# Kernel optimization log

Measured on AMD Instinct MI355X. Metric: run time of the kernel, lower is better.

## Reference

```python
import jax, jax.numpy as jnp
import numpy as np

HEAD_DIM = 256
L2_EPS = 1e-12  # tf.math.l2_normalize default epsilon


def setup_inputs() -> dict:
    key = jax.random.key(0)
    ks = jax.random.split(key, 6)
    B, U = 64, 2048
    D_dec, D_enc = 1024, 512
    H, K, A = 4, HEAD_DIM, 1024
    s = 0.075  # RandomUniform(-0.075, 0.075) kernel init
    return {
        "dec_state": jax.random.normal(ks[0], (B, D_dec), jnp.float32),
        "enc_state": jax.random.normal(ks[1], (B, U, D_enc), jnp.float32),
        "phi_w": jax.random.uniform(ks[2], (H, D_dec, K), jnp.float32, -s, s),
        "phi_b": jnp.zeros((H, K), jnp.float32),
        "psi_w": jax.random.uniform(ks[3], (H, D_enc, K), jnp.float32, -s, s),
        "psi_b": jnp.zeros((H, K), jnp.float32),
        "out_w": jax.random.uniform(ks[4], (H * D_enc, A), jnp.float32, -s, s),
        "out_b": jnp.zeros((A,), jnp.float32),
    }


def reference(dec_state, enc_state, phi_w, phi_b, psi_w, psi_b, out_w, out_b):
    B = dec_state.shape[0]
    # Per-head query/key projections, all heads at once.
    phi_s = jnp.einsum("bd,hdk->bhk", dec_state, phi_w) + phi_b[None]      # (B,H,K)
    psi_h = jnp.einsum("bue,hek->bhuk", enc_state, psi_w) + psi_b[None, :, None]  # (B,H,U,K)
    scale = 1.0 / jnp.sqrt(jnp.asarray(HEAD_DIM, jnp.float32))
    energy = jnp.einsum("bhk,bhuk->bhu", phi_s, psi_h) * scale              # (B,H,U)
    attn = jax.nn.softmax(energy, axis=-1)
    # NOTE: the original attends over the RAW enc_state (not psi_h).
    ctx = jnp.einsum("bhu,bue->bhe", attn, enc_state)                        # (B,H,E)
    # tf.math.l2_normalize over last axis
    sq = jnp.sum(ctx * ctx, axis=-1, keepdims=True)
    ctx = ctx * jax.lax.rsqrt(jnp.maximum(sq, L2_EPS))
    combined = ctx.reshape(B, -1)                                            # (B, H*E) == concat over heads
    return combined @ out_w + out_b
```

## Files before the change

### kernel.cpp

```cpp
#include <hip/hip_runtime.h>
#include <math.h>

typedef float f2 __attribute__((ext_vector_type(2)));

constexpr int NB = 64;
constexpr int NU = 2048;
constexpr int ND = 1024;
constexpr int NE = 512;
constexpr int NH = 4;
constexpr int NK = 256;
constexpr int NA = 1024;
constexpr int NS = 16;
constexpr int ROWS_PER_BLOCK = NU / NS;
constexpr int ROWS_PER_WAVE  = ROWS_PER_BLOCK / 4;
constexpr float SCALE = 0.0625f;

constexpr int RSPLIT = 16;
constexpr int RCH = (NH*NE)/RSPLIT;
constexpr int BT = 8;

constexpr int DSP = 16;

constexpr size_t WS_Q   = 0;
constexpr size_t WS_CTX = WS_Q + (size_t)NB*NH*NE;
constexpr size_t WS_P   = WS_CTX + (size_t)NB*NH*NE;

__global__ __launch_bounds__(256) void k_phi(
    const float* __restrict__ dec, const float* __restrict__ phi_w,
    float* __restrict__ P, float* __restrict__ q, float* __restrict__ ctxacc,
    const float* __restrict__ out_b, float* __restrict__ out)
{
  const int flat = blockIdx.x;
  const int kc = flat & 3;
  const int h  = (flat >> 2) & 3;
  const int ds = flat >> 4;
  const int t = threadIdx.x;

  ctxacc[(size_t)flat*512 + t]       = 0.f;
  ctxacc[(size_t)flat*512 + 256 + t] = 0.f;
  q[(size_t)flat*512 + t]            = 0.f;
  q[(size_t)flat*512 + 256 + t]      = 0.f;
  out[(size_t)flat*256 + t] = out_b[(flat*256 + t) & (NA-1)];

  const int d0 = ds*64, k0 = kc*64;

  __shared__ float phi_lds[64][64];
  __shared__ float dec_t[64][68];

  {
    const int kq = t & 15, r = t >> 4;
    const float* pwb = phi_w + ((size_t)h*ND + d0)*NK + k0;
    #pragma unroll
    for (int p = 0; p < 4; ++p) {
      float4 v = *(const float4*)(pwb + (size_t)(r + 16*p)*NK + 4*kq);
      *(float4*)&phi_lds[r + 16*p][4*kq] = v;
    }
    const float* db = dec + d0 + 4*kq;
    #pragma unroll
    for (int p = 0; p < 4; ++p) {
      const int b = r + 16*p;
      float4 v = *(const float4*)(db + (size_t)b*ND);
      dec_t[4*kq+0][b] = v.x; dec_t[4*kq+1][b] = v.y;
      dec_t[4*kq+2][b] = v.z; dec_t[4*kq+3][b] = v.w;
    }
  }
  __syncthreads();

  const int k = t & 63, bq = t >> 6, b0 = bq*16;
  f2 acc2[8];
  #pragma unroll
  for (int i = 0; i < 8; ++i) acc2[i] = f2{0.f, 0.f};
  #pragma unroll 4
  for (int d = 0; d < 64; ++d) {
    float w = phi_lds[d][k];
    f2 ww = f2{w, w};
    float4 a0 = *(const float4*)&dec_t[d][b0];
    float4 a1 = *(const float4*)&dec_t[d][b0+4];
    float4 a2 = *(const float4*)&dec_t[d][b0+8];
    float4 a3 = *(const float4*)&dec_t[d][b0+12];
    acc2[0] += f2{a0.x,a0.y}*ww; acc2[1] += f2{a0.z,a0.w}*ww;
    acc2[2] += f2{a1.x,a1.y}*ww; acc2[3] += f2{a1.z,a1.w}*ww;
    acc2[4] += f2{a2.x,a2.y}*ww; acc2[5] += f2{a2.z,a2.w}*ww;
    acc2[6] += f2{a3.x,a3.y}*ww; acc2[7] += f2{a3.z,a3.w}*ww;
  }
  float* pb = P + (((size_t)ds*64 + b0)*NH + h)*NK + k0 + k;
  #pragma unroll
  for (int j = 0; j < 8; ++j) {
    pb[(size_t)(2*j  )*NH*NK] = acc2[j][0];
    pb[(size_t)(2*j+1)*NH*NK] = acc2[j][1];
  }
}

__global__ __launch_bounds__(256) void k_q(
    const float* __restrict__ P, const float* __restrict__ phi_b,
    const float* __restrict__ psi_w, float* __restrict__ q)
{
  const int flat = blockIdx.x;
  const int ks = flat & 3;
  const int ec = (flat >> 2) & 7;
  const int h  = flat >> 5;
  const int t = threadIdx.x;
  const int k0 = ks*64, e0 = ec*64;

  __shared__ float phi_red[64][68];
  __shared__ float psi_lds[64][65];

  {
    const int e = t >> 2, kq4 = t & 3;
    const float* pb = psi_w + ((size_t)h*NE + e0 + e)*NK + k0 + 4*kq4;
    #pragma unroll
    for (int p = 0; p < 4; ++p) {
      float4 v = *(const float4*)(pb + 16*p);
      const int kk = 4*(kq4 + 4*p);
      psi_lds[e][kk+0] = v.x; psi_lds[e][kk+1] = v.y;
      psi_lds[e][kk+2] = v.z; psi_lds[e][kk+3] = v.w;
    }
  }
  {
    const int b = t >> 2, kq4 = t & 3;
    const float* pbase = P + ((size_t)b*NH + h)*NK + k0 + 4*kq4;
    #pragma unroll
    for (int p = 0; p < 4; ++p) {
      float4 s = make_float4(0.f, 0.f, 0.f, 0.f);
      #pragma unroll
      for (int dsi = 0; dsi < DSP; ++dsi) {
        float4 v = *(const float4*)(pbase + (size_t)dsi*64*NH*NK + 16*p);
        s.x += v.x; s.y += v.y; s.z += v.z; s.w += v.w;
      }
      const int kk = 4*(kq4 + 4*p);
      const float* bb = phi_b + h*NK + k0 + kk;
      phi_red[kk+0][b] = s.x + bb[0];
      phi_red[kk+1][b] = s.y + bb[1];
      phi_red[kk+2][b] = s.z + bb[2];
      phi_red[kk+3][b] = s.w + bb[3];
    }
  }
  __syncthreads();

  const int e = t & 63, bq = t >> 6, b0 = bq*16;
  f2 acc2[8];
  #pragma unroll
  for (int i = 0; i < 8; ++i) acc2[i] = f2{0.f, 0.f};
  #pragma unroll 4
  for (int kl = 0; kl < 64; ++kl) {
    float w = psi_lds[e][kl];
    f2 ww = f2{w, w};
    float4 a0 = *(const float4*)&phi_red[kl][b0];
    float4 a1 = *(const float4*)&phi_red[kl][b0+4];
    float4 a2 = *(const float4*)&phi_red[kl][b0+8];
    float4 a3 = *(const float4*)&phi_red[kl][b0+12];
    acc2[0] += f2{a0.x,a0.y}*ww; acc2[1] += f2{a0.z,a0.w}*ww;
    acc2[2] += f2{a1.x,a1.y}*ww; acc2[3] += f2{a1.z,a1.w}*ww;
    acc2[4] += f2{a2.x,a2.y}*ww; acc2[5] += f2{a2.z,a2.w}*ww;
    acc2[6] += f2{a3.x,a3.y}*ww; acc2[7] += f2{a3.z,a3.w}*ww;
  }
  float* qb = q + ((size_t)b0*NH + h)*NE + e0 + e;
  #pragma unroll
  for (int j = 0; j < 8; ++j) {
    unsafeAtomicAdd(qb + (size_t)(2*j  )*NH*NE, acc2[j][0]);
    unsafeAtomicAdd(qb + (size_t)(2*j+1)*NH*NE, acc2[j][1]);
  }
}

__global__ __launch_bounds__(256, 4) void k_flash(
    const float* __restrict__ enc, const float* __restrict__ qg,
    float* __restrict__ ctxacc)
{
  const int s = blockIdx.x;
  const int b = blockIdx.y;
  const int t = threadIdx.x;
  const int wave = t >> 6;
  const int lane = t & 63;

  f2 qv[NH][4];
  const float* qb = qg + (size_t)b*NH*NE;
  #pragma unroll
  for (int h = 0; h < NH; ++h) {
    float4 a0 = *(const float4*)(qb + h*NE + 4*lane);
    float4 a1 = *(const float4*)(qb + h*NE + 256 + 4*lane);
    qv[h][0] = f2{a0.x, a0.y}; qv[h][1] = f2{a0.z, a0.w};
    qv[h][2] = f2{a1.x, a1.y}; qv[h][3] = f2{a1.z, a1.w};
  }
  f2 acc2[NH][4];
  #pragma unroll
  for (int h = 0; h < NH; ++h)
    #pragma unroll
    for (int j = 0; j < 4; ++j) acc2[h][j] = f2{0.f, 0.f};

  const int u0 = s*ROWS_PER_BLOCK + wave*ROWS_PER_WAVE;
  const float* encb = enc + ((size_t)b*NU + u0)*NE;
  #pragma unroll 2
  for (int r = 0; r < ROWS_PER_WAVE; ++r) {
    float4 v0 = *(const float4*)(encb + (size_t)r*NE + 4*lane);
    float4 v1 = *(const float4*)(encb + (size_t)r*NE + 256 + 4*lane);
    f2 e0 = f2{v0.x, v0.y}, e1 = f2{v0.z, v0.w};
    f2 e2 = f2{v1.x, v1.y}, e3 = f2{v1.z, v1.w};
    float d[NH];
    #pragma unroll
    for (int h = 0; h < NH; ++h) {
      f2 p = e0*qv[h][0] + e1*qv[h][1] + e2*qv[h][2] + e3*qv[h][3];
      d[h] = p[0] + p[1];
    }
    #pragma unroll
    for (int off = 1; off < 64; off <<= 1) {
      #pragma unroll
      for (int h = 0; h < NH; ++h) d[h] += __shfl_xor(d[h], off);
    }
    #pragma unroll
    for (int h = 0; h < NH; ++h) {
      float pf = __expf(d[h] * SCALE);
      f2 pp = f2{pf, pf};
      acc2[h][0] += pp*e0; acc2[h][1] += pp*e1;
      acc2[h][2] += pp*e2; acc2[h][3] += pp*e3;
    }
  }
  __shared__ float acc_lds[4][NH][NE];
  #pragma unroll
  for (int h = 0; h < NH; ++h) {
    *(float4*)&acc_lds[wave][h][4*lane] =
        make_float4(acc2[h][0][0], acc2[h][0][1], acc2[h][1][0], acc2[h][1][1]);
    *(float4*)&acc_lds[wave][h][256 + 4*lane] =
        make_float4(acc2[h][2][0], acc2[h][2][1], acc2[h][3][0], acc2[h][3][1]);
  }
  __syncthreads();
  float* cb = ctxacc + (size_t)b*(NH*NE);
  #pragma unroll
  for (int h = 0; h < NH; ++h) {
    #pragma unroll
    for (int eo = 0; eo < 2; ++eo) {
      int e = t + eo*256;
      float v = acc_lds[0][h][e] + acc_lds[1][h][e] + acc_lds[2][h][e] + acc_lds[3][h][e];
      unsafeAtomicAdd(&cb[h*NE + e], v);
    }
  }
}

__global__ __launch_bounds__(256) void k_out(
    const float* __restrict__ ctxacc, const float* __restrict__ out_w,
    float* __restrict__ out)
{
  const int t = threadIdx.x;
  const int a = blockIdx.x*256 + t;
  const int b0 = blockIdx.y * BT;
  const int rc = blockIdx.z;
  const int h  = rc >> 2;
  const int e0 = (rc & 3) * RCH;

  __shared__ float rn_lds[BT];
  const int wv = t >> 6, lane = t & 63;
  {
    const int i = 2*wv + (lane >> 5);
    const int l32 = lane & 31;
    const float* row = ctxacc + (size_t)(b0+i)*(NH*NE) + (size_t)h*NE;
    float ss = 0.f;
    #pragma unroll
    for (int j = 0; j < 16; ++j) { float v = row[l32 + 32*j]; ss += v*v; }
    #pragma unroll
    for (int off = 1; off < 32; off <<= 1) ss += __shfl_xor(ss, off);
    if (l32 == 0) rn_lds[i] = rsqrtf(fmaxf(ss, 1e-12f));
  }
  __syncthreads();

  __shared__ float c_lds[RCH][BT];
  for (int g = t; g < RCH*BT; g += 256) {
    const int r = g & (RCH-1), i = g >> 7;
    c_lds[r][i] = ctxacc[(size_t)(b0+i)*(NH*NE) + (size_t)h*NE + e0 + r] * rn_lds[i];
  }
  __syncthreads();

  float accv[BT];
  #pragma unroll
  for (int i = 0; i < BT; ++i) accv[i] = 0.f;
  const float* w = out_w + ((size_t)rc*RCH)*NA + a;
  #pragma unroll 8
  for (int r = 0; r < RCH; ++r) {
    float wvv = w[(size_t)r*NA];
    float4 ca = *(const float4*)&c_lds[r][0];
    float4 cb = *(const float4*)&c_lds[r][4];
    accv[0] += ca.x*wvv; accv[1] += ca.y*wvv; accv[2] += ca.z*wvv; accv[3] += ca.w*wvv;
    accv[4] += cb.x*wvv; accv[5] += cb.y*wvv; accv[6] += cb.z*wvv; accv[7] += cb.w*wvv;
  }
  #pragma unroll
  for (int i = 0; i < BT; ++i)
    unsafeAtomicAdd(&out[(size_t)(b0+i)*NA + a], accv[i]);
}

extern "C" void kernel_launch(void* const* d_in, const int* in_sizes, int n_in,
                              void* d_out, int out_size, void* d_ws, size_t ws_size,
                              hipStream_t stream) {
  const float* dec   = (const float*)d_in[0];
  const float* enc   = (const float*)d_in[1];
  const float* phi_w = (const float*)d_in[2];
  const float* phi_b = (const float*)d_in[3];
  const float* psi_w = (const float*)d_in[4];
  const float* out_w = (const float*)d_in[6];
  const float* out_b = (const float*)d_in[7];
  float* out = (float*)d_out;
  float* ws = (float*)d_ws;
  float* q      = ws + WS_Q;
  float* ctxacc = ws + WS_CTX;
  float* P      = ws + WS_P;

  hipLaunchKernelGGL(k_phi,   dim3(NH*4*DSP),              dim3(256), 0, stream,
                     dec, phi_w, P, q, ctxacc, out_b, out);
  hipLaunchKernelGGL(k_q,     dim3(128),                   dim3(256), 0, stream,
                     P, phi_b, psi_w, q);
  hipLaunchKernelGGL(k_flash, dim3(NS, NB),                dim3(256), 0, stream,
                     enc, q, ctxacc);
  hipLaunchKernelGGL(k_out,   dim3(NA/256, NB/BT, RSPLIT), dim3(256), 0, stream,
                     ctxacc, out_w, out);
}
```

Measured before the change: 84.71 us.

## Restructure flash kernel: one wave per head, half-wave per row, double-buffered loads

The attention kernel now assigns one wave per head instead of one wave per row slice. Each half-wave processes one encoder row, so a wave covers two rows per step. Each block's waves all stream the same rows (one per head) with double-buffered register loads and periodic barriers to keep them in lockstep for cache sharing. This removes the LDS cross-wave reduction and cuts the shuffle reduction to 5 steps, and the scale is pre-folded into q. In exchange, each row is loaded four times (once per head wave), which relies on L1/L2 hits, and the occupancy hint in launch_bounds is dropped.

New measurement: 102.7 us. +21.3%, slower.

```diff
diff --git a/kernel.cpp b/kernel.cpp
--- a/kernel.cpp
+++ b/kernel.cpp
@@ -12,7 +12,6 @@
 constexpr int NA = 1024;
 constexpr int NS = 16;
 constexpr int ROWS_PER_BLOCK = NU / NS;
-constexpr int ROWS_PER_WAVE  = ROWS_PER_BLOCK / 4;
 constexpr float SCALE = 0.0625f;
 
 constexpr int RSPLIT = 16;
@@ -162,75 +161,85 @@
   }
 }
 
-__global__ __launch_bounds__(256, 4) void k_flash(
+__device__ __forceinline__ f2 shflx(f2 v, int m) {
+  return f2{__shfl_xor(v[0], m), __shfl_xor(v[1], m)};
+}
+
+__global__ __launch_bounds__(256) void k_flash(
     const float* __restrict__ enc, const float* __restrict__ qg,
     float* __restrict__ ctxacc)
 {
   const int s = blockIdx.x;
   const int b = blockIdx.y;
   const int t = threadIdx.x;
-  const int wave = t >> 6;
+  const int h = t >> 6;
   const int lane = t & 63;
-
-  f2 qv[NH][4];
-  const float* qb = qg + (size_t)b*NH*NE;
-  #pragma unroll
-  for (int h = 0; h < NH; ++h) {
-    float4 a0 = *(const float4*)(qb + h*NE + 4*lane);
-    float4 a1 = *(const float4*)(qb + h*NE + 256 + 4*lane);
-    qv[h][0] = f2{a0.x, a0.y}; qv[h][1] = f2{a0.z, a0.w};
-    qv[h][2] = f2{a1.x, a1.y}; qv[h][3] = f2{a1.z, a1.w};
-  }
-  f2 acc2[NH][4];
-  #pragma unroll
-  for (int h = 0; h < NH; ++h)
-    #pragma unroll
-    for (int j = 0; j < 4; ++j) acc2[h][j] = f2{0.f, 0.f};
-
-  const int u0 = s*ROWS_PER_BLOCK + wave*ROWS_PER_WAVE;
-  const float* encb = enc + ((size_t)b*NU + u0)*NE;
-  #pragma unroll 2
-  for (int r = 0; r < ROWS_PER_WAVE; ++r) {
-    float4 v0 = *(const float4*)(encb + (size_t)r*NE + 4*lane);
-    float4 v1 = *(const float4*)(encb + (size_t)r*NE + 256 + 4*lane);
-    f2 e0 = f2{v0.x, v0.y}, e1 = f2{v0.z, v0.w};
-    f2 e2 = f2{v1.x, v1.y}, e3 = f2{v1.z, v1.w};
-    float d[NH];
-    #pragma unroll
-    for (int h = 0; h < NH; ++h) {
-      f2 p = e0*qv[h][0] + e1*qv[h][1] + e2*qv[h][2] + e3*qv[h][3];
-      d[h] = p[0] + p[1];
-    }
-    #pragma unroll
-    for (int off = 1; off < 64; off <<= 1) {
-      #pragma unroll
-      for (int h = 0; h < NH; ++h) d[h] += __shfl_xor(d[h], off);
-    }
-    #pragma unroll
-    for (int h = 0; h < NH; ++h) {
-      float pf = __expf(d[h] * SCALE);
-      f2 pp = f2{pf, pf};
-      acc2[h][0] += pp*e0; acc2[h][1] += pp*e1;
-      acc2[h][2] += pp*e2; acc2[h][3] += pp*e3;
-    }
-  }
-  __shared__ float acc_lds[4][NH][NE];
-  #pragma unroll
-  for (int h = 0; h < NH; ++h) {
-    *(float4*)&acc_lds[wave][h][4*lane] =
-        make_float4(acc2[h][0][0], acc2[h][0][1], acc2[h][1][0], acc2[h][1][1]);
-    *(float4*)&acc_lds[wave][h][256 + 4*lane] =
-        make_float4(acc2[h][2][0], acc2[h][2][1], acc2[h][3][0], acc2[h][3][1]);
-  }
-  __syncthreads();
-  float* cb = ctxacc + (size_t)b*(NH*NE);
-  #pragma unroll
-  for (int h = 0; h < NH; ++h) {
-    #pragma unroll
-    for (int eo = 0; eo < 2; ++eo) {
-      int e = t + eo*256;
-      float v = acc_lds[0][h][e] + acc_lds[1][h][e] + acc_lds[2][h][e] + acc_lds[3][h][e];
-      unsafeAtomicAdd(&cb[h*NE + e], v);
+  const int half = lane >> 5;
+  const int l32 = lane & 31;
+
+  f2 qv[8];
+  const float* qbase = qg + ((size_t)b*NH + h)*NE + 4*l32;
+  #pragma unroll
+  for (int ch = 0; ch < 4; ++ch) {
+    float4 a = *(const float4*)(qbase + ch*128);
+    qv[2*ch]   = f2{a.x*SCALE, a.y*SCALE};
+    qv[2*ch+1] = f2{a.z*SCALE, a.w*SCALE};
+  }
+
+  f2 acc[8];
+  #pragma unroll
+  for (int j = 0; j < 8; ++j) acc[j] = f2{0.f, 0.f};
+
+  const float* myrow = enc + ((size_t)b*NU + s*ROWS_PER_BLOCK + half)*NE + 4*l32;
+
+#define LOADP(r_, p_) { \
+    const float* rp_ = myrow + (size_t)(p_)*2*NE; \
+    r_[0] = *(const float4*)(rp_);       r_[1] = *(const float4*)(rp_ + 128); \
+    r_[2] = *(const float4*)(rp_ + 256); r_[3] = *(const float4*)(rp_ + 384); }
+
+#define COMPP(x_) { \
+    f2 xf[8]; \
+    xf[0]=f2{x_[0].x,x_[0].y}; xf[1]=f2{x_[0].z,x_[0].w}; \
+    xf[2]=f2{x_[1].x,x_[1].y}; xf[3]=f2{x_[1].z,x_[1].w}; \
+    xf[4]=f2{x_[2].x,x_[2].y}; xf[5]=f2{x_[2].z,x_[2].w}; \
+    xf[6]=f2{x_[3].x,x_[3].y}; xf[7]=f2{x_[3].z,x_[3].w}; \
+    f2 pr = xf[0]*qv[0]; \
+    _Pragma("unroll") \
+    for (int j = 1; j < 8; ++j) pr += xf[j]*qv[j]; \
+    float d = pr[0] + pr[1]; \
+    d += __shfl_xor(d, 1);  d += __shfl_xor(d, 2);  d += __shfl_xor(d, 4); \
+    d += __shfl_xor(d, 8);  d += __shfl_xor(d, 16); \
+    float w = __expf(d); \
+    f2 ww = f2{w, w}; \
+    _Pragma("unroll") \
+    for (int j = 0; j < 8; ++j) acc[j] += ww*xf[j]; }
+
+  constexpr int NP = ROWS_PER_BLOCK/2;
+  float4 A[4], B[4];
+  LOADP(A, 0) LOADP(B, 1)
+  #pragma unroll 4
+  for (int i = 0; i < NP; i += 2) {
+    if ((i & 3) == 0) __builtin_amdgcn_s_barrier();
+    COMPP(A)
+    if (i + 2 < NP) LOADP(A, i + 2)
+    COMPP(B)
+    if (i + 3 < NP) LOADP(B, i + 3)
+  }
+#undef LOADP
+#undef COMPP
+
+  #pragma unroll
+  for (int j = 0; j < 8; ++j) acc[j] += shflx(acc[j], 32);
+
+  float* cb = ctxacc + ((size_t)b*NH + h)*NE;
+  if (half == 0) {
+    #pragma unroll
+    for (int ch = 0; ch < 4; ++ch) {
+      const int e = ch*128 + 4*l32;
+      unsafeAtomicAdd(&cb[e+0], acc[2*ch][0]);
+      unsafeAtomicAdd(&cb[e+1], acc[2*ch][1]);
+      unsafeAtomicAdd(&cb[e+2], acc[2*ch+1][0]);
+      unsafeAtomicAdd(&cb[e+3], acc[2*ch+1][1]);
     }
   }
 }
```
